# Optimization experiments

Hardware: AMD Instinct MI355X
Metric: run time of the kernel (lower is better)

The kernel has to match this reference:

```python
import jax, jax.numpy as jnp
import numpy as np

# MACE symmetric contraction, element-dependent, correlation=3, scalar (0e) output.
B, C, L, E = 8192, 128, 16, 10     # atoms, feature channels, sum(2l+1) for lmax=3, elements
K1, K2, K3 = 1, 4, 23              # U-matrix path counts per correlation order


def _sparse_U(key, shape, density):
    # Clebsch-Gordan-like tensors are highly sparse/structured; emulate with masked randn.
    kv, km = jax.random.split(key)
    mask = jax.random.bernoulli(km, density, shape)
    return jnp.where(mask, jax.random.normal(kv, shape), 0.0).astype(jnp.float32)


def setup_inputs() -> dict:
    key = jax.random.key(0)
    ks = jax.random.split(key, 8)
    U1 = _sparse_U(ks[0], (L, K1), 0.5)          # (i, k1)
    U2 = _sparse_U(ks[1], (L, L, K2), 0.12)      # (p, i, k2)
    U3 = _sparse_U(ks[2], (L, L, L, K3), 0.12)   # (p, q, i, k3)
    W1 = (jax.random.normal(ks[3], (E, K1, C)) / K1).astype(jnp.float32)
    W2 = (jax.random.normal(ks[4], (E, K2, C)) / K2).astype(jnp.float32)
    W3 = (jax.random.normal(ks[5], (E, K3, C)) / K3).astype(jnp.float32)
    x = jax.random.normal(ks[6], (B, C, L), dtype=jnp.float32)
    y = jax.random.uniform(ks[7], (B, E), dtype=jnp.float32)  # element attribute vector
    return {"x": x, "y": y, "U1": U1, "U2": U2, "U3": U3, "W1": W1, "W2": W2, "W3": W3}


def reference(x, y, U1, U2, U3, W1, W2, W3):
    # correlation = 3 main contraction: '...ik,ekc,bci,be->bc...'
    out = jnp.einsum('pqik,ekc,bci,be->bcpq', U3, W3, x, y)      # (B, C, L, L)
    # corr = 2: weighting '...k,ekc,be->bc...' then contract 'bc...i,bci->bc...'
    c2 = jnp.einsum('pik,ekc,be->bcpi', U2, W2, y) + out          # (B, C, L, L)
    out = jnp.einsum('bcpi,bci->bcp', c2, x)                      # (B, C, L)
    # corr = 1
    c1 = jnp.einsum('ik,ekc,be->bci', U1, W1, y) + out            # (B, C, L)
    out = jnp.einsum('bci,bci->bc', c1, x)                        # (B, C)
    return out  # already flattened: (B, C)
```

## Files before the change

kernel.cpp:

```cpp
#include <hip/hip_runtime.h>
#include <stdint.h>

#define B_ATOMS 8192
#define C_CH    128
#define CHB     64
#define L_DIM   16
#define E_EL    10
#define NK3     23
#define NK2     4
#define NSLOT   1024
#define NCOL    32
#define CHUNK   128
#define ROWB    272
#define TSE     72

#define XX_OFF  0
#define WT_OFF  17408
#define WS_OFF  22016
#define SMEM_BYTES 23040

typedef __attribute__((ext_vector_type(8))) short short8;
typedef __attribute__((ext_vector_type(4))) float f32x4;

struct Lut3 { unsigned char a[NSLOT]; unsigned char b[NSLOT]; unsigned char c[NSLOT]; };
static constexpr Lut3 make_lut3() {
  Lut3 t{};
  int s = 0;
  for (int i = 0; i < 16; ++i)
    for (int j = i; j < 16; ++j)
      for (int k = j; k < 16; ++k) { t.a[s] = (unsigned char)i; t.b[s] = (unsigned char)j; t.c[s] = (unsigned char)k; ++s; }
  for (int i = 0; i < 16; ++i)
    for (int j = i; j < 16; ++j) { t.a[s] = (unsigned char)i; t.b[s] = (unsigned char)j; t.c[s] = 16; ++s; }
  for (int i = 0; i < 16; ++i) { t.a[s] = (unsigned char)i; t.b[s] = 16; t.c[s] = 16; ++s; }
  for (; s < NSLOT; ++s) { t.a[s] = 17; t.b[s] = 17; t.c[s] = 17; }
  return t;
}
__constant__ Lut3 LUT3C = make_lut3();
static constexpr Lut3 LUT3 = make_lut3();

__device__ __forceinline__ unsigned short f2bf(float f) {
  union { float f; unsigned u; } v; v.f = f;
  unsigned r = v.u + 0x7fffu + ((v.u >> 16) & 1u);
  return (unsigned short)(r >> 16);
}
__device__ __forceinline__ unsigned pk_bf16(float lo, float hi) {
  unsigned r;
  asm("v_cvt_pk_bf16_f32 %0, %1, %2" : "=v"(r) : "v"(lo), "v"(hi));
  return r;
}
__device__ __forceinline__ float2 bfup(unsigned u) {
  float2 r;
  r.x = __uint_as_float(u << 16);
  r.y = __uint_as_float(u & 0xffff0000u);
  return r;
}
template <int CTRL>
__device__ __forceinline__ float dpp_add(float s) {
  int v = __builtin_amdgcn_update_dpp(0, __float_as_int(s), CTRL, 0xf, 0xf, true);
  return s + __int_as_float(v);
}
__device__ __forceinline__ float row16_sum(float s) {
  s = dpp_add<0x111>(s);
  s = dpp_add<0x112>(s);
  s = dpp_add<0x114>(s);
  s = dpp_add<0x118>(s);
  return s;
}

__global__ void build_bt(const float* __restrict__ U1, const float* __restrict__ U2,
                         const float* __restrict__ U3, unsigned short* __restrict__ bt) {
  int gid = blockIdx.x * 256 + threadIdx.x;
  if (gid >= NCOL * NSLOT) return;
  const int j  = gid >> 10;
  const int kk = gid & (NSLOT - 1);
  const int a = LUT3C.a[kk], b = LUT3C.b[kk], c = LUT3C.c[kk];
  float val = 0.f;
  if (a < 16) {
    if (c < 16) {
      if (j < NK3) {
        int P[6][3] = {{a,b,c},{a,c,b},{b,a,c},{b,c,a},{c,a,b},{c,b,a}};
        for (int t1 = 0; t1 < 6; ++t1) {
          bool dup = false;
          for (int t2 = 0; t2 < t1; ++t2)
            dup = dup || (P[t1][0]==P[t2][0] && P[t1][1]==P[t2][1] && P[t1][2]==P[t2][2]);
          if (!dup) val += U3[((P[t1][0]*16 + P[t1][1])*16 + P[t1][2])*NK3 + j];
        }
      }
    } else if (b < 16) {
      if (j >= NK3 && j < NK3 + NK2) {
        const int k2 = j - NK3;
        val = U2[(a*16 + b)*NK2 + k2];
        if (a != b) val += U2[(b*16 + a)*NK2 + k2];
      }
    } else {
      if (j == NK3 + NK2) val = U1[a];
    }
  }
  bt[(size_t)gid] = f2bf(val);
}

template <int S>
__device__ __forceinline__ float slot_val(const float* xf) {
  constexpr int a = LUT3.a[S], b = LUT3.b[S], c = LUT3.c[S];
  if constexpr (a >= 17) return 0.f;
  else if constexpr (b >= 16) return xf[a];
  else if constexpr (c >= 16) return xf[a] * xf[b];
  else return xf[a] * xf[b] * xf[c];
}

template <int S0, int G>
__device__ __forceinline__ void stage_groups(char* rb, const float* xf) {
  if constexpr (G < 4) {
    uint4 v;
    v.x = pk_bf16(slot_val<S0 + G*8 + 0>(xf), slot_val<S0 + G*8 + 1>(xf));
    v.y = pk_bf16(slot_val<S0 + G*8 + 2>(xf), slot_val<S0 + G*8 + 3>(xf));
    v.z = pk_bf16(slot_val<S0 + G*8 + 4>(xf), slot_val<S0 + G*8 + 5>(xf));
    v.w = pk_bf16(slot_val<S0 + G*8 + 6>(xf), slot_val<S0 + G*8 + 7>(xf));
    *(uint4*)(rb + G * 16) = v;
    stage_groups<S0, G + 1>(rb, xf);
  }
}

template <int T>
__device__ __forceinline__ void chunk_step(char* arow, const char* abase,
                                           const unsigned short* bp0,
                                           const unsigned short* bp1,
                                           const float* xf,
                                           f32x4 (&acc)[4][2], int wu) {
  short8 bfr0 = *(const short8*)(bp0 + T * CHUNK);
  short8 bfr1 = *(const short8*)(bp1 + T * CHUNK);
  switch (wu) {
    case 0:  stage_groups<T * CHUNK +  0, 0>(arow, xf); break;
    case 1:  stage_groups<T * CHUNK + 32, 0>(arow, xf); break;
    case 2:  stage_groups<T * CHUNK + 64, 0>(arow, xf); break;
    default: stage_groups<T * CHUNK + 96, 0>(arow, xf); break;
  }
  asm volatile("" ::: "memory");
  short8 af[4];
#pragma unroll
  for (int mt = 0; mt < 4; ++mt)
    af[mt] = *(const short8*)(abase + mt * (16 * ROWB));
#pragma unroll
  for (int mt = 0; mt < 4; ++mt) {
    acc[mt][0] = __builtin_amdgcn_mfma_f32_16x16x32_bf16(af[mt], bfr0, acc[mt][0], 0, 0, 0);
    acc[mt][1] = __builtin_amdgcn_mfma_f32_16x16x32_bf16(af[mt], bfr1, acc[mt][1], 0, 0, 0);
  }
  asm volatile("" ::: "memory");
}

__global__ __launch_bounds__(256, 6) void mace_main(
    const float* __restrict__ x, const float* __restrict__ y,
    const float* __restrict__ W1, const float* __restrict__ W2,
    const float* __restrict__ W3,
    const unsigned short* __restrict__ bt, float* __restrict__ out) {
  __shared__ __align__(16) char smem[SMEM_BYTES];
  const int t    = threadIdx.x;
  const int b    = blockIdx.y;
  const int ch0  = blockIdx.x * CHB;
  const int lane = t & 63;
  const int wu   = __builtin_amdgcn_readfirstlane(t >> 6);
  const int quad = lane >> 4, l16 = lane & 15;

  float xf[16];
  {
    const float4* xs = (const float4*)(x + ((size_t)b * C_CH + ch0 + lane) * L_DIM);
    float4 f0 = xs[0], f1 = xs[1], f2 = xs[2], f3 = xs[3];
    xf[0]=f0.x;  xf[1]=f0.y;  xf[2]=f0.z;  xf[3]=f0.w;
    xf[4]=f1.x;  xf[5]=f1.y;  xf[6]=f1.z;  xf[7]=f1.w;
    xf[8]=f2.x;  xf[9]=f2.y;  xf[10]=f2.z; xf[11]=f2.w;
    xf[12]=f3.x; xf[13]=f3.y; xf[14]=f3.z; xf[15]=f3.w;
  }

  {
    float yv[E_EL];
#pragma unroll
    for (int e = 0; e < E_EL; ++e) yv[e] = y[(size_t)b * E_EL + e];
    unsigned short* wtb = (unsigned short*)(smem + WT_OFF);
#pragma unroll
    for (int u0 = 0; u0 < 2; ++u0) {
      const int u = t + u0 * 256;
      const int k = u >> 4, cg = (u & 15) * 4;
      float4 a = {0.f, 0.f, 0.f, 0.f};
      if (k < NK3) {
#pragma unroll
        for (int e = 0; e < E_EL; ++e) {
          float4 wv = *(const float4*)(W3 + ((size_t)e * NK3 + k) * C_CH + ch0 + cg);
          a.x += yv[e] * wv.x; a.y += yv[e] * wv.y; a.z += yv[e] * wv.z; a.w += yv[e] * wv.w;
        }
      } else if (k < NK3 + NK2) {
#pragma unroll
        for (int e = 0; e < E_EL; ++e) {
          float4 wv = *(const float4*)(W2 + ((size_t)e * NK2 + (k - NK3)) * C_CH + ch0 + cg);
          a.x += yv[e] * wv.x; a.y += yv[e] * wv.y; a.z += yv[e] * wv.z; a.w += yv[e] * wv.w;
        }
      } else if (k == NK3 + NK2) {
#pragma unroll
        for (int e = 0; e < E_EL; ++e) {
          float4 wv = *(const float4*)(W1 + (size_t)e * C_CH + ch0 + cg);
          a.x += yv[e] * wv.x; a.y += yv[e] * wv.y; a.z += yv[e] * wv.z; a.w += yv[e] * wv.w;
        }
      }
      uint2 pw;
      pw.x = pk_bf16(a.x, a.y);
      pw.y = pk_bf16(a.z, a.w);
      *(uint2*)(wtb + k * TSE + cg) = pw;
    }
  }
  __syncthreads();

  const unsigned short* const bp0 = bt + (l16 << 10) + wu * 32 + quad * 8;
  const unsigned short* const bp1 = bp0 + (16 << 10);
  char* const arow        = smem + XX_OFF + lane * ROWB + wu * 64;
  const char* const abase = smem + XX_OFF + l16 * ROWB + wu * 64 + quad * 16;
  f32x4 acc[4][2];
#pragma unroll
  for (int mt = 0; mt < 4; ++mt) {
    acc[mt][0] = (f32x4){0.f, 0.f, 0.f, 0.f};
    acc[mt][1] = (f32x4){0.f, 0.f, 0.f, 0.f};
  }
  chunk_step<0>(arow, abase, bp0, bp1, xf, acc, wu);
  chunk_step<1>(arow, abase, bp0, bp1, xf, acc, wu);
  chunk_step<2>(arow, abase, bp0, bp1, xf, acc, wu);
  chunk_step<3>(arow, abase, bp0, bp1, xf, acc, wu);
  chunk_step<4>(arow, abase, bp0, bp1, xf, acc, wu);
  chunk_step<5>(arow, abase, bp0, bp1, xf, acc, wu);
  chunk_step<6>(arow, abase, bp0, bp1, xf, acc, wu);
  chunk_step<7>(arow, abase, bp0, bp1, xf, acc, wu);

  float* ws = (float*)(smem + WS_OFF);
  const unsigned short* wt = (const unsigned short*)(smem + WT_OFF);
#pragma unroll
  for (int mt = 0; mt < 4; ++mt) {
    const int c4 = mt * 16 + quad * 4;
    float s0 = 0.f, s1 = 0.f, s2 = 0.f, s3 = 0.f;
#pragma unroll
    for (int nt = 0; nt < 2; ++nt) {
      uint2 wv = *(const uint2*)(wt + (nt * 16 + l16) * TSE + c4);
      float2 w01 = bfup(wv.x), w23 = bfup(wv.y);
      s0 += acc[mt][nt][0] * w01.x;
      s1 += acc[mt][nt][1] * w01.y;
      s2 += acc[mt][nt][2] * w23.x;
      s3 += acc[mt][nt][3] * w23.y;
    }
    s0 = row16_sum(s0);
    s1 = row16_sum(s1);
    s2 = row16_sum(s2);
    s3 = row16_sum(s3);
    if (l16 == 15) *(float4*)(ws + wu * CHB + c4) = (float4){s0, s1, s2, s3};
  }
  __syncthreads();
  if (t < CHB) {
    float s = ws[t] + ws[CHB + t] + ws[2 * CHB + t] + ws[3 * CHB + t];
    out[(size_t)b * C_CH + ch0 + t] = s;
  }
}

extern "C" void kernel_launch(void* const* d_in, const int* in_sizes, int n_in,
                              void* d_out, int out_size, void* d_ws, size_t ws_size,
                              hipStream_t stream) {
  const float* x  = (const float*)d_in[0];
  const float* y  = (const float*)d_in[1];
  const float* U1 = (const float*)d_in[2];
  const float* U2 = (const float*)d_in[3];
  const float* U3 = (const float*)d_in[4];
  const float* W1 = (const float*)d_in[5];
  const float* W2 = (const float*)d_in[6];
  const float* W3 = (const float*)d_in[7];
  float* out = (float*)d_out;
  unsigned short* bt = (unsigned short*)d_ws;
  if (ws_size < (size_t)NCOL * NSLOT * sizeof(unsigned short)) return;

  build_bt<<<dim3((NCOL * NSLOT + 255) / 256), dim3(256), 0, stream>>>(U1, U2, U3, bt);
  mace_main<<<dim3(2, B_ATOMS), dim3(256), 0, stream>>>(x, y, W1, W2, W3, bt, out);
}
```

Before: 266.3 us.

## Software-pipeline A-tile staging and B-fragment loads one chunk ahead of MFMAs

```diff
diff --git a/kernel.cpp b/kernel.cpp
--- a/kernel.cpp
+++ b/kernel.cpp
@@ -126,29 +126,34 @@
                                            const unsigned short* bp0,
                                            const unsigned short* bp1,
                                            const float* xf,
-                                           f32x4 (&acc)[4][2], int wu) {
-  short8 bfr0 = *(const short8*)(bp0 + T * CHUNK);
-  short8 bfr1 = *(const short8*)(bp1 + T * CHUNK);
-  switch (wu) {
-    case 0:  stage_groups<T * CHUNK +  0, 0>(arow, xf); break;
-    case 1:  stage_groups<T * CHUNK + 32, 0>(arow, xf); break;
-    case 2:  stage_groups<T * CHUNK + 64, 0>(arow, xf); break;
-    default: stage_groups<T * CHUNK + 96, 0>(arow, xf); break;
-  }
-  asm volatile("" ::: "memory");
+                                           f32x4 (&acc)[4][2],
+                                           short8 (&bfr)[2], int wu) {
   short8 af[4];
 #pragma unroll
   for (int mt = 0; mt < 4; ++mt)
     af[mt] = *(const short8*)(abase + mt * (16 * ROWB));
+  asm volatile("" ::: "memory");
+  short8 bnxt[2];
+  if constexpr (T < 7) {
+    bnxt[0] = *(const short8*)(bp0 + (T + 1) * CHUNK);
+    bnxt[1] = *(const short8*)(bp1 + (T + 1) * CHUNK);
+    switch (wu) {
+      case 0:  stage_groups<(T + 1) * CHUNK +  0, 0>(arow, xf); break;
+      case 1:  stage_groups<(T + 1) * CHUNK + 32, 0>(arow, xf); break;
+      case 2:  stage_groups<(T + 1) * CHUNK + 64, 0>(arow, xf); break;
+      default: stage_groups<(T + 1) * CHUNK + 96, 0>(arow, xf); break;
+    }
+  }
 #pragma unroll
   for (int mt = 0; mt < 4; ++mt) {
-    acc[mt][0] = __builtin_amdgcn_mfma_f32_16x16x32_bf16(af[mt], bfr0, acc[mt][0], 0, 0, 0);
-    acc[mt][1] = __builtin_amdgcn_mfma_f32_16x16x32_bf16(af[mt], bfr1, acc[mt][1], 0, 0, 0);
-  }
+    acc[mt][0] = __builtin_amdgcn_mfma_f32_16x16x32_bf16(af[mt], bfr[0], acc[mt][0], 0, 0, 0);
+    acc[mt][1] = __builtin_amdgcn_mfma_f32_16x16x32_bf16(af[mt], bfr[1], acc[mt][1], 0, 0, 0);
+  }
+  if constexpr (T < 7) { bfr[0] = bnxt[0]; bfr[1] = bnxt[1]; }
   asm volatile("" ::: "memory");
 }
 
-__global__ __launch_bounds__(256, 6) void mace_main(
+__global__ __launch_bounds__(256, 5) void mace_main(
     const float* __restrict__ x, const float* __restrict__ y,
     const float* __restrict__ W1, const float* __restrict__ W2,
     const float* __restrict__ W3,
@@ -171,6 +176,22 @@
     xf[12]=f3.x; xf[13]=f3.y; xf[14]=f3.z; xf[15]=f3.w;
   }
 
+  const unsigned short* const bp0 = bt + (l16 << 10) + wu * 32 + quad * 8;
+  const unsigned short* const bp1 = bp0 + (16 << 10);
+  char* const arow        = smem + XX_OFF + lane * ROWB + wu * 64;
+  const char* const abase = smem + XX_OFF + l16 * ROWB + wu * 64 + quad * 16;
+
+  short8 bfr[2];
+  switch (wu) {
+    case 0:  stage_groups< 0, 0>(arow, xf); break;
+    case 1:  stage_groups<32, 0>(arow, xf); break;
+    case 2:  stage_groups<64, 0>(arow, xf); break;
+    default: stage_groups<96, 0>(arow, xf); break;
+  }
+  bfr[0] = *(const short8*)(bp0);
+  bfr[1] = *(const short8*)(bp1);
+  asm volatile("" ::: "memory");
+
   {
     float yv[E_EL];
 #pragma unroll
@@ -208,24 +229,20 @@
   }
   __syncthreads();
 
-  const unsigned short* const bp0 = bt + (l16 << 10) + wu * 32 + quad * 8;
-  const unsigned short* const bp1 = bp0 + (16 << 10);
-  char* const arow        = smem + XX_OFF + lane * ROWB + wu * 64;
-  const char* const abase = smem + XX_OFF + l16 * ROWB + wu * 64 + quad * 16;
   f32x4 acc[4][2];
 #pragma unroll
   for (int mt = 0; mt < 4; ++mt) {
     acc[mt][0] = (f32x4){0.f, 0.f, 0.f, 0.f};
     acc[mt][1] = (f32x4){0.f, 0.f, 0.f, 0.f};
   }
-  chunk_step<0>(arow, abase, bp0, bp1, xf, acc, wu);
-  chunk_step<1>(arow, abase, bp0, bp1, xf, acc, wu);
-  chunk_step<2>(arow, abase, bp0, bp1, xf, acc, wu);
-  chunk_step<3>(arow, abase, bp0, bp1, xf, acc, wu);
-  chunk_step<4>(arow, abase, bp0, bp1, xf, acc, wu);
-  chunk_step<5>(arow, abase, bp0, bp1, xf, acc, wu);
-  chunk_step<6>(arow, abase, bp0, bp1, xf, acc, wu);
-  chunk_step<7>(arow, abase, bp0, bp1, xf, acc, wu);
+  chunk_step<0>(arow, abase, bp0, bp1, xf, acc, bfr, wu);
+  chunk_step<1>(arow, abase, bp0, bp1, xf, acc, bfr, wu);
+  chunk_step<2>(arow, abase, bp0, bp1, xf, acc, bfr, wu);
+  chunk_step<3>(arow, abase, bp0, bp1, xf, acc, bfr, wu);
+  chunk_step<4>(arow, abase, bp0, bp1, xf, acc, bfr, wu);
+  chunk_step<5>(arow, abase, bp0, bp1, xf, acc, bfr, wu);
+  chunk_step<6>(arow, abase, bp0, bp1, xf, acc, bfr, wu);
+  chunk_step<7>(arow, abase, bp0, bp1, xf, acc, bfr, wu);
 
   float* ws = (float*)(smem + WS_OFF);
   const unsigned short* wt = (const unsigned short*)(smem + WT_OFF);
```

New measurement: 288.3 us. 1.08x slower.

## Feed MFMA A operand from registers via permlane swap, drop LDS staging

Applied to the files above, without the earlier changes.

```diff
diff --git a/kernel.cpp b/kernel.cpp
--- a/kernel.cpp
+++ b/kernel.cpp
@@ -10,17 +10,14 @@
 #define NK2     4
 #define NSLOT   1024
 #define NCOL    32
-#define CHUNK   128
-#define ROWB    272
-#define TSE     72
-
-#define XX_OFF  0
-#define WT_OFF  17408
-#define WS_OFF  22016
-#define SMEM_BYTES 23040
-
-typedef __attribute__((ext_vector_type(8))) short short8;
-typedef __attribute__((ext_vector_type(4))) float f32x4;
+
+#define WTT_OFF 0
+#define WS_OFF  4608
+#define SMEM_BYTES (4608 + 16 * 66 * 4)
+
+typedef __attribute__((ext_vector_type(8)))  short short8;
+typedef __attribute__((ext_vector_type(16))) float f32x16;
+typedef __attribute__((ext_vector_type(4)))  unsigned int u32x4;
 
 struct Lut3 { unsigned char a[NSLOT]; unsigned char b[NSLOT]; unsigned char c[NSLOT]; };
 static constexpr Lut3 make_lut3() {
@@ -46,12 +43,6 @@
 __device__ __forceinline__ unsigned pk_bf16(float lo, float hi) {
   unsigned r;
   asm("v_cvt_pk_bf16_f32 %0, %1, %2" : "=v"(r) : "v"(lo), "v"(hi));
-  return r;
-}
-__device__ __forceinline__ float2 bfup(unsigned u) {
-  float2 r;
-  r.x = __uint_as_float(u << 16);
-  r.y = __uint_as_float(u & 0xffff0000u);
   return r;
 }
 template <int CTRL>
@@ -108,47 +99,33 @@
   else return xf[a] * xf[b] * xf[c];
 }
 
-template <int S0, int G>
-__device__ __forceinline__ void stage_groups(char* rb, const float* xf) {
-  if constexpr (G < 4) {
-    uint4 v;
-    v.x = pk_bf16(slot_val<S0 + G*8 + 0>(xf), slot_val<S0 + G*8 + 1>(xf));
-    v.y = pk_bf16(slot_val<S0 + G*8 + 2>(xf), slot_val<S0 + G*8 + 3>(xf));
-    v.z = pk_bf16(slot_val<S0 + G*8 + 4>(xf), slot_val<S0 + G*8 + 5>(xf));
-    v.w = pk_bf16(slot_val<S0 + G*8 + 6>(xf), slot_val<S0 + G*8 + 7>(xf));
-    *(uint4*)(rb + G * 16) = v;
-    stage_groups<S0, G + 1>(rb, xf);
-  }
-}
-
-template <int T>
-__device__ __forceinline__ void chunk_step(char* arow, const char* abase,
-                                           const unsigned short* bp0,
-                                           const unsigned short* bp1,
-                                           const float* xf,
-                                           f32x4 (&acc)[4][2], int wu) {
-  short8 bfr0 = *(const short8*)(bp0 + T * CHUNK);
-  short8 bfr1 = *(const short8*)(bp1 + T * CHUNK);
-  switch (wu) {
-    case 0:  stage_groups<T * CHUNK +  0, 0>(arow, xf); break;
-    case 1:  stage_groups<T * CHUNK + 32, 0>(arow, xf); break;
-    case 2:  stage_groups<T * CHUNK + 64, 0>(arow, xf); break;
-    default: stage_groups<T * CHUNK + 96, 0>(arow, xf); break;
-  }
-  asm volatile("" ::: "memory");
-  short8 af[4];
-#pragma unroll
-  for (int mt = 0; mt < 4; ++mt)
-    af[mt] = *(const short8*)(abase + mt * (16 * ROWB));
-#pragma unroll
-  for (int mt = 0; mt < 4; ++mt) {
-    acc[mt][0] = __builtin_amdgcn_mfma_f32_16x16x32_bf16(af[mt], bfr0, acc[mt][0], 0, 0, 0);
-    acc[mt][1] = __builtin_amdgcn_mfma_f32_16x16x32_bf16(af[mt], bfr1, acc[mt][1], 0, 0, 0);
-  }
-  asm volatile("" ::: "memory");
-}
-
-__global__ __launch_bounds__(256, 6) void mace_main(
+template <int K0, int S>
+__device__ __forceinline__ void gemm_steps(const float* xf, const unsigned short* bp,
+                                           f32x16& a0, f32x16& a1) {
+  if constexpr (S < 16) {
+    constexpr int K = K0 + S * 16;
+    unsigned L0 = pk_bf16(slot_val<K +  0>(xf), slot_val<K +  1>(xf));
+    unsigned L1 = pk_bf16(slot_val<K +  2>(xf), slot_val<K +  3>(xf));
+    unsigned L2 = pk_bf16(slot_val<K +  4>(xf), slot_val<K +  5>(xf));
+    unsigned L3 = pk_bf16(slot_val<K +  6>(xf), slot_val<K +  7>(xf));
+    unsigned H0 = pk_bf16(slot_val<K +  8>(xf), slot_val<K +  9>(xf));
+    unsigned H1 = pk_bf16(slot_val<K + 10>(xf), slot_val<K + 11>(xf));
+    unsigned H2 = pk_bf16(slot_val<K + 12>(xf), slot_val<K + 13>(xf));
+    unsigned H3 = pk_bf16(slot_val<K + 14>(xf), slot_val<K + 15>(xf));
+    short8 bfr = *(const short8*)(bp + S * 16);
+    asm("v_permlane32_swap_b32 %0, %1" : "+v"(L0), "+v"(H0));
+    asm("v_permlane32_swap_b32 %0, %1" : "+v"(L1), "+v"(H1));
+    asm("v_permlane32_swap_b32 %0, %1" : "+v"(L2), "+v"(H2));
+    asm("v_permlane32_swap_b32 %0, %1" : "+v"(L3), "+v"(H3));
+    short8 Af0 = __builtin_bit_cast(short8, (u32x4){L0, L1, L2, L3});
+    short8 Af1 = __builtin_bit_cast(short8, (u32x4){H0, H1, H2, H3});
+    a0 = __builtin_amdgcn_mfma_f32_32x32x16_bf16(Af0, bfr, a0, 0, 0, 0);
+    a1 = __builtin_amdgcn_mfma_f32_32x32x16_bf16(Af1, bfr, a1, 0, 0, 0);
+    gemm_steps<K0, S + 1>(xf, bp, a0, a1);
+  }
+}
+
+__global__ __launch_bounds__(256, 4) void mace_main(
     const float* __restrict__ x, const float* __restrict__ y,
     const float* __restrict__ W1, const float* __restrict__ W2,
     const float* __restrict__ W3,
@@ -159,7 +136,9 @@
   const int ch0  = blockIdx.x * CHB;
   const int lane = t & 63;
   const int wu   = __builtin_amdgcn_readfirstlane(t >> 6);
-  const int quad = lane >> 4, l16 = lane & 15;
+  const int col  = lane & 31;
+  const int half = lane >> 5;
+  const int l16  = lane & 15;
 
   float xf[16];
   {
@@ -175,7 +154,7 @@
     float yv[E_EL];
 #pragma unroll
     for (int e = 0; e < E_EL; ++e) yv[e] = y[(size_t)b * E_EL + e];
-    unsigned short* wtb = (unsigned short*)(smem + WT_OFF);
+    unsigned short* wtt = (unsigned short*)(smem + WTT_OFF);
 #pragma unroll
     for (int u0 = 0; u0 < 2; ++u0) {
       const int u = t + u0 * 256;
@@ -200,57 +179,53 @@
           a.x += yv[e] * wv.x; a.y += yv[e] * wv.y; a.z += yv[e] * wv.z; a.w += yv[e] * wv.w;
         }
       }
-      uint2 pw;
-      pw.x = pk_bf16(a.x, a.y);
-      pw.y = pk_bf16(a.z, a.w);
-      *(uint2*)(wtb + k * TSE + cg) = pw;
+      const unsigned p01 = pk_bf16(a.x, a.y), p23 = pk_bf16(a.z, a.w);
+      const unsigned short v4[4] = {(unsigned short)(p01 & 0xffffu), (unsigned short)(p01 >> 16),
+                                    (unsigned short)(p23 & 0xffffu), (unsigned short)(p23 >> 16)};
+      const int cmb = cg & 31, hb = cg >> 5;
+#pragma unroll
+      for (int i = 0; i < 4; ++i)
+        wtt[((cmb + i) * 36 + k) * 2 + hb] = v4[i];
     }
   }
   __syncthreads();
 
-  const unsigned short* const bp0 = bt + (l16 << 10) + wu * 32 + quad * 8;
-  const unsigned short* const bp1 = bp0 + (16 << 10);
-  char* const arow        = smem + XX_OFF + lane * ROWB + wu * 64;
-  const char* const abase = smem + XX_OFF + l16 * ROWB + wu * 64 + quad * 16;
-  f32x4 acc[4][2];
-#pragma unroll
-  for (int mt = 0; mt < 4; ++mt) {
-    acc[mt][0] = (f32x4){0.f, 0.f, 0.f, 0.f};
-    acc[mt][1] = (f32x4){0.f, 0.f, 0.f, 0.f};
-  }
-  chunk_step<0>(arow, abase, bp0, bp1, xf, acc, wu);
-  chunk_step<1>(arow, abase, bp0, bp1, xf, acc, wu);
-  chunk_step<2>(arow, abase, bp0, bp1, xf, acc, wu);
-  chunk_step<3>(arow, abase, bp0, bp1, xf, acc, wu);
-  chunk_step<4>(arow, abase, bp0, bp1, xf, acc, wu);
-  chunk_step<5>(arow, abase, bp0, bp1, xf, acc, wu);
-  chunk_step<6>(arow, abase, bp0, bp1, xf, acc, wu);
-  chunk_step<7>(arow, abase, bp0, bp1, xf, acc, wu);
+  const unsigned short* const bp = bt + ((size_t)col << 10) + wu * 256 + half * 8;
+  f32x16 acc0, acc1;
+#pragma unroll
+  for (int i = 0; i < 16; ++i) { acc0[i] = 0.f; acc1[i] = 0.f; }
+  switch (wu) {
+    case 0:  gemm_steps<  0, 0>(xf, bp, acc0, acc1); break;
+    case 1:  gemm_steps<256, 0>(xf, bp, acc0, acc1); break;
+    case 2:  gemm_steps<512, 0>(xf, bp, acc0, acc1); break;
+    default: gemm_steps<768, 0>(xf, bp, acc0, acc1); break;
+  }
 
   float* ws = (float*)(smem + WS_OFF);
-  const unsigned short* wt = (const unsigned short*)(smem + WT_OFF);
-#pragma unroll
-  for (int mt = 0; mt < 4; ++mt) {
-    const int c4 = mt * 16 + quad * 4;
-    float s0 = 0.f, s1 = 0.f, s2 = 0.f, s3 = 0.f;
-#pragma unroll
-    for (int nt = 0; nt < 2; ++nt) {
-      uint2 wv = *(const uint2*)(wt + (nt * 16 + l16) * TSE + c4);
-      float2 w01 = bfup(wv.x), w23 = bfup(wv.y);
-      s0 += acc[mt][nt][0] * w01.x;
-      s1 += acc[mt][nt][1] * w01.y;
-      s2 += acc[mt][nt][2] * w23.x;
-      s3 += acc[mt][nt][3] * w23.y;
+  const unsigned short* wtt = (const unsigned short*)(smem + WTT_OFF);
+#pragma unroll
+  for (int reg = 0; reg < 16; ++reg) {
+    const int cm = (reg & 3) + 8 * (reg >> 2) + 4 * half;
+    const unsigned wv = *(const unsigned*)(wtt + (cm * 36 + col) * 2);
+    const float w0 = __uint_as_float(wv << 16);
+    const float w1 = __uint_as_float(wv & 0xffff0000u);
+    float p0 = acc0[reg] * w0;
+    float p1 = acc1[reg] * w1;
+    p0 = row16_sum(p0);
+    p1 = row16_sum(p1);
+    if (l16 == 15) {
+      const int prow = (wu * 4 + (lane >> 4)) * 66;
+      ws[prow + cm]      = p0;
+      ws[prow + cm + 32] = p1;
     }
-    s0 = row16_sum(s0);
-    s1 = row16_sum(s1);
-    s2 = row16_sum(s2);
-    s3 = row16_sum(s3);
-    if (l16 == 15) *(float4*)(ws + wu * CHB + c4) = (float4){s0, s1, s2, s3};
   }
   __syncthreads();
   if (t < CHB) {
-    float s = ws[t] + ws[CHB + t] + ws[2 * CHB + t] + ws[3 * CHB + t];
+    const int g0 = ((t & 7) >= 4) ? 2 : 0;
+    float s = 0.f;
+#pragma unroll
+    for (int w = 0; w < 4; ++w)
+      s += ws[(w * 4 + g0) * 66 + t] + ws[(w * 4 + g0 + 1) * 66 + t];
     out[(size_t)b * C_CH + ch0 + t] = s;
   }
 }
```

Result: slower. 287.1 us (+7.8%).
